# Optimization experiments

Hardware: AMD Instinct MI355X
Metric: run time of the kernel (lower is better)

## Reference

```python
import jax, jax.numpy as jnp
import numpy as np

TOLERANCE = 0.01  # init kwarg


def setup_inputs() -> dict:
    key = jax.random.key(0)
    k1, k2 = jax.random.split(key)
    B, N = 64, 2048
    logits = jax.random.normal(k1, (B, N), dtype=jnp.float32)
    labels = jax.random.uniform(k2, (B, N), dtype=jnp.float32)
    return {"logits": logits, "labels": labels}


def reference(logits, labels):
    # Original: for each row, sort labels descending; for every ordered pair
    # (high, low) in that order with |label_high - label_low| > tolerance,
    # accumulate log(sigmoid(logit_high - logit_low)); reduction='sum' per
    # row, then mean over the batch.
    # Vectorized equivalent: a pair contributes iff labels[a] - labels[b] > tol
    # (exactly one ordering per unordered pair, ties masked out).
    label_diff = labels[:, :, None] - labels[:, None, :]          # [B, N, N]
    mask = label_diff > TOLERANCE                                  # [B, N, N]
    logit_diff = logits[:, :, None] - logits[:, None, :]          # [B, N, N]
    log_sig = jax.nn.log_sigmoid(logit_diff)
    per_row = jnp.sum(jnp.where(mask, log_sig, 0.0), axis=(1, 2))  # [B]
    return jnp.mean(per_row)
```

## Files before the change

### kernel.cpp

```cpp
#include <hip/hip_runtime.h>
#include <math.h>


#define NN 2048
#define BB 64
#define TOLF 0.01f
#define BLK 256
#define NTILE 20
#define TILEBLKS (BB * NTILE)
#define SIDEBLKS (BB * 8)
#define WGRID (TILEBLKS + SIDEBLKS)
#define SWIN 448
#define LOG2E 1.4426950408889634f

typedef float v2f __attribute__((ext_vector_type(2)));

__device__ float2 g_labs[BB][NN];
__device__ float  g_Es[BB][NN];
__device__ int    g_C[BB][NN];
__device__ float  g_part[TILEBLKS];
__device__ double g_partS[SIDEBLKS];

__global__ __launch_bounds__(BLK) void rank_pre(const float* __restrict__ logits,
                                                const float* __restrict__ labels) {
    __shared__ float2 sls[NN];
    __shared__ float  sEv[NN];
    __shared__ int    sC[NN];
    __shared__ int    cnt[100], pref[101], offs[100];
    __shared__ int    wtot;
    const int row = blockIdx.x, tid = threadIdx.x;
    const float* lg = logits + (size_t)row * NN;
    const float* lb = labels + (size_t)row * NN;

    for (int x = tid; x < 100; x += BLK) { cnt[x] = 0; offs[x] = 0; }
    __syncthreads();

    int   myb[8];
    float myla[8], mylg[8];
#pragma unroll
    for (int q = 0; q < 8; ++q) {
        int x = tid + q * BLK;
        myla[q] = lb[x];
        mylg[q] = lg[x];
        myb[q]  = min(99, (int)(myla[q] * 100.0f));
        atomicAdd(&cnt[myb[q]], 1);
    }
    __syncthreads();
    {
        int v = (tid < 100) ? cnt[tid] : 0;
        int x = v;
#pragma unroll
        for (int o = 1; o < 64; o <<= 1) {
            int y = __shfl_up(x, o);
            if ((tid & 63) >= o) x += y;
        }
        if (tid == 63) wtot = x;
        __syncthreads();
        if (tid >= 64 && tid < 128) x += wtot;
        if (tid < 101) pref[tid] = x - v;
    }
    __syncthreads();
#pragma unroll
    for (int q = 0; q < 8; ++q) {
        int b = myb[q];
        int p = pref[b] + atomicAdd(&offs[b], 1);
        float s = mylg[q] * LOG2E;
        sls[p] = make_float2(myla[q], s);
        sEv[p] = __builtin_amdgcn_exp2f(s);
        sC[p]  = (b >= 1) ? pref[b - 1] : 0;
    }
    __syncthreads();
    for (int x = tid; x < NN; x += BLK) {
        g_labs[row][x] = sls[x];
        g_Es[row][x]   = sEv[x];
        g_C[row][x]    = sC[x];
    }
}

__global__ __launch_bounds__(BLK) void rank_work() {
    const int bid = blockIdx.x;
    if (bid < SIDEBLKS) {
        __shared__ float2 sLS[SWIN];
        __shared__ float  sE[SWIN];
        __shared__ int    sCs;
        __shared__ double sdw[4];
        const int row = bid >> 3;
        const int c0  = (bid & 7) << 8;
        const int tid = threadIdx.x;
        if (tid == 0) sCs = g_C[row][c0];
        __syncthreads();
        const int Cs  = sCs;
        const int len = c0 + 256 - Cs;
        for (int x = tid; x < len; x += BLK) {
            sLS[x] = g_labs[row][Cs + x];
            sE[x]  = g_Es[row][Cs + x];
        }
        __syncthreads();

        const int i    = c0 + tid;
        const int iloc = i - Cs;
        const float2 lsi = sLS[iloc];
        const float lai = lsi.x, si = lsi.y;
        const float Ei  = sE[iloc];
        const int wloc  = g_C[row][i] - Cs;

        float accL = 0.0f, accS = 0.0f;
        float p = 1.0f;
        int cnt8 = 0;
        for (int j = wloc; j < iloc; ++j) {
            float2 ls = sLS[j];
            float ld = lai - ls.x;
            bool valid = fabsf(ld) > TOLF;
            float term = valid ? (Ei + sE[j]) : 1.0f;
            p *= term;
            if (++cnt8 == 8) { accL += __builtin_amdgcn_logf(p); p = 1.0f; cnt8 = 0; }
            float sh = (ld > 0.0f) ? si : ls.y;
            accS -= valid ? sh : 0.0f;
        }
        accL += __builtin_amdgcn_logf(p);

        double acc = (double)accL + (double)accS;
        for (int off = 32; off > 0; off >>= 1) acc += __shfl_down(acc, off);
        if ((tid & 63) == 0) sdw[tid >> 6] = acc;
        __syncthreads();
        if (tid == 0) g_partS[bid] = sdw[0] + sdw[1] + sdw[2] + sdw[3];
    } else {
        __shared__ __align__(16) float swin[256];
        __shared__ float swave[4];
        const int tb = bid - SIDEBLKS;
        const int row = tb / NTILE;
        const int t = tb % NTILE;
        const int it = (t < 2) ? 0 : (t < 6) ? 1 : (t < 12) ? 2 : 3;
        const int jt = t - it * (it + 1);
        const int ibeg = it * 512, jbeg = jt * 256;

        float accL = 0.0f;
        const int Cmax = g_C[row][ibeg + 511];
        if (jbeg < Cmax) {
            for (int x = threadIdx.x; x < 64; x += BLK)
                ((float4*)swin)[x] = ((const float4*)&g_Es[row][jbeg])[x];
            __syncthreads();
            const int ia = ibeg + threadIdx.x;
            const int ib = ia + 256;
            const float invEa = __builtin_amdgcn_rcpf(g_Es[row][ia]);
            const float invEb = __builtin_amdgcn_rcpf(g_Es[row][ib]);
            v2f iA; iA.x = invEa; iA.y = invEa;
            v2f iB; iB.x = invEb; iB.y = invEb;
            int tripa = max(0, min(256, g_C[row][ia] - jbeg));
            int tripb = max(0, min(256, g_C[row][ib] - jbeg));
            const int m16a = tripa & ~15;
            const int m16b = tripb & ~15;

            for (int jj = 0; jj < m16a; jj += 16) {
                const v2f* qw = (const v2f*)&swin[jj];
                v2f a0; a0.x = 1.0f; a0.y = 1.0f;
                v2f a1 = a0, b0 = a0, b1 = a0;
#pragma unroll
                for (int u = 0; u < 4; ++u) {
                    v2f w = qw[u];
                    a0 = __builtin_elementwise_fma(w * iA, a0, a0);
                    b0 = __builtin_elementwise_fma(w * iB, b0, b0);
                }
#pragma unroll
                for (int u = 4; u < 8; ++u) {
                    v2f w = qw[u];
                    a1 = __builtin_elementwise_fma(w * iA, a1, a1);
                    b1 = __builtin_elementwise_fma(w * iB, b1, b1);
                }
                accL += __builtin_amdgcn_logf(a0.x * a0.y)
                      + __builtin_amdgcn_logf(a1.x * a1.y)
                      + __builtin_amdgcn_logf(b0.x * b0.y)
                      + __builtin_amdgcn_logf(b1.x * b1.y);
            }
            for (int jj = m16a; jj < m16b; jj += 16) {
                const v2f* qw = (const v2f*)&swin[jj];
                v2f b0; b0.x = 1.0f; b0.y = 1.0f;
                v2f b1 = b0;
#pragma unroll
                for (int u = 0; u < 4; ++u)
                    b0 = __builtin_elementwise_fma(qw[u] * iB, b0, b0);
#pragma unroll
                for (int u = 4; u < 8; ++u)
                    b1 = __builtin_elementwise_fma(qw[u] * iB, b1, b1);
                accL += __builtin_amdgcn_logf(b0.x * b0.y)
                      + __builtin_amdgcn_logf(b1.x * b1.y);
            }
            if (m16a < tripa) {
                float p0 = 1.0f, p1 = 1.0f;
#pragma unroll
                for (int u = 0; u < 8; ++u) {
                    float t0 = (m16a + u     < tripa) ? fmaf(swin[m16a + u],     invEa, 1.0f) : 1.0f;
                    float t1 = (m16a + 8 + u < tripa) ? fmaf(swin[m16a + 8 + u], invEa, 1.0f) : 1.0f;
                    p0 *= t0; p1 *= t1;
                }
                accL += __builtin_amdgcn_logf(p0) + __builtin_amdgcn_logf(p1);
            }
            if (m16b < tripb) {
                float p0 = 1.0f, p1 = 1.0f;
#pragma unroll
                for (int u = 0; u < 8; ++u) {
                    float t0 = (m16b + u     < tripb) ? fmaf(swin[m16b + u],     invEb, 1.0f) : 1.0f;
                    float t1 = (m16b + 8 + u < tripb) ? fmaf(swin[m16b + 8 + u], invEb, 1.0f) : 1.0f;
                    p0 *= t0; p1 *= t1;
                }
                accL += __builtin_amdgcn_logf(p0) + __builtin_amdgcn_logf(p1);
            }
        }
        for (int off = 32; off > 0; off >>= 1) accL += __shfl_down(accL, off);
        if ((threadIdx.x & 63) == 0) swave[threadIdx.x >> 6] = accL;
        __syncthreads();
        if (threadIdx.x == 0)
            g_part[tb] = swave[0] + swave[1] + swave[2] + swave[3];
    }
}

__global__ __launch_bounds__(BLK) void rank_final(float* __restrict__ out) {
    double acc = 0.0;
    for (int idx = threadIdx.x; idx < TILEBLKS; idx += BLK) acc += (double)g_part[idx];
    for (int idx = threadIdx.x; idx < SIDEBLKS; idx += BLK) acc += g_partS[idx];
    for (int off = 32; off > 0; off >>= 1) acc += __shfl_down(acc, off);
    __shared__ double sw[4];
    if ((threadIdx.x & 63) == 0) sw[threadIdx.x >> 6] = acc;
    __syncthreads();
    if (threadIdx.x == 0)
        out[0] = (float)((sw[0] + sw[1] + sw[2] + sw[3]) *
                         (-0.6931471805599453 / (double)BB));
}

extern "C" void kernel_launch(void* const* d_in, const int* in_sizes, int n_in,
                              void* d_out, int out_size, void* d_ws, size_t ws_size,
                              hipStream_t stream) {
    const float* logits = (const float*)d_in[0];
    const float* labels = (const float*)d_in[1];
    float* out = (float*)d_out;
    (void)in_sizes; (void)n_in; (void)out_size; (void)d_ws; (void)ws_size;

    rank_pre<<<BB, BLK, 0, stream>>>(logits, labels);
    rank_work<<<WGRID, BLK, 0, stream>>>();
    rank_final<<<1, BLK, 0, stream>>>(out);
}
```

Measured before the change: 26.64 us.

## Fuse preprocessing and pairwise work kernels with per-row ready flags

Merges the per-row bucket-sort preprocessing kernel and the pairwise work kernel into one launch. The first 64 blocks sort rows and publish a release flag, and worker blocks spin on that flag with acquire loads before processing. Each worker now handles two items in successive passes, and exp values and bucket starts are packed into a single float2 array to cut separate loads. This removes one launch gap and lets work overlap with preprocessing of other rows. It depends on the producer blocks being scheduled, which risks deadlock if resident capacity is exceeded, and it adds spin-wait overhead and halves worker parallelism.

```diff
diff --git a/kernel.cpp b/kernel.cpp
--- a/kernel.cpp
+++ b/kernel.cpp
@@ -9,208 +9,234 @@
 #define NTILE 20
 #define TILEBLKS (BB * NTILE)
 #define SIDEBLKS (BB * 8)
-#define WGRID (TILEBLKS + SIDEBLKS)
+#define NITEMS (TILEBLKS + SIDEBLKS)
+#define WBLKS (NITEMS / 2)
+#define GRID (BB + WBLKS)
 #define SWIN 448
 #define LOG2E 1.4426950408889634f
 
 typedef float v2f __attribute__((ext_vector_type(2)));
 
 __device__ float2 g_labs[BB][NN];
-__device__ float  g_Es[BB][NN];
-__device__ int    g_C[BB][NN];
+__device__ float2 g_EC[BB][NN];
+__device__ int    g_ready[BB * 16];
 __device__ float  g_part[TILEBLKS];
 __device__ double g_partS[SIDEBLKS];
 
-__global__ __launch_bounds__(BLK) void rank_pre(const float* __restrict__ logits,
-                                                const float* __restrict__ labels) {
-    __shared__ float2 sls[NN];
-    __shared__ float  sEv[NN];
-    __shared__ int    sC[NN];
-    __shared__ int    cnt[100], pref[101], offs[100];
-    __shared__ int    wtot;
-    const int row = blockIdx.x, tid = threadIdx.x;
-    const float* lg = logits + (size_t)row * NN;
-    const float* lb = labels + (size_t)row * NN;
-
-    for (int x = tid; x < 100; x += BLK) { cnt[x] = 0; offs[x] = 0; }
-    __syncthreads();
-
-    int   myb[8];
-    float myla[8], mylg[8];
-#pragma unroll
-    for (int q = 0; q < 8; ++q) {
-        int x = tid + q * BLK;
-        myla[q] = lb[x];
-        mylg[q] = lg[x];
-        myb[q]  = min(99, (int)(myla[q] * 100.0f));
-        atomicAdd(&cnt[myb[q]], 1);
+#define SMEM_BYTES 17664
+
+__global__ __launch_bounds__(BLK, 4) void rank_fused(const float* __restrict__ logits,
+                                                     const float* __restrict__ labels) {
+    __shared__ __align__(16) char smem[SMEM_BYTES];
+    const int bid = blockIdx.x, tid = threadIdx.x;
+
+    if (bid < BB) {
+        float2* st = (float2*)smem;
+        int* cnt  = (int*)(smem + 16384);
+        int* offs = cnt + 100;
+        int* pref = offs + 100;
+        int* wtot = pref + 101;
+        const int row = bid;
+        const float* lg = logits + (size_t)row * NN;
+        const float* lb = labels + (size_t)row * NN;
+
+        for (int x = tid; x < 100; x += BLK) { cnt[x] = 0; offs[x] = 0; }
+        __syncthreads();
+        float la8[8], lg8[8];
+        int   p8[8];
+#pragma unroll
+        for (int q = 0; q < 8; ++q) {
+            int x = tid + q * BLK;
+            la8[q] = lb[x];
+            lg8[q] = lg[x];
+            atomicAdd(&cnt[min(99, (int)(la8[q] * 100.0f))], 1);
+        }
+        __syncthreads();
+        {
+            int v = (tid < 100) ? cnt[tid] : 0;
+            int x = v;
+#pragma unroll
+            for (int o = 1; o < 64; o <<= 1) {
+                int y = __shfl_up(x, o);
+                if ((tid & 63) >= o) x += y;
+            }
+            if (tid == 63) *wtot = x;
+            __syncthreads();
+            if (tid >= 64 && tid < 128) x += *wtot;
+            if (tid < 101) pref[tid] = x - v;
+        }
+        __syncthreads();
+#pragma unroll
+        for (int q = 0; q < 8; ++q) {
+            int b = min(99, (int)(la8[q] * 100.0f));
+            p8[q] = pref[b] + atomicAdd(&offs[b], 1);
+            st[p8[q]] = make_float2(la8[q], lg8[q] * LOG2E);
+        }
+        __syncthreads();
+        for (int x = tid; x < NN; x += BLK) g_labs[row][x] = st[x];
+        __syncthreads();
+#pragma unroll
+        for (int q = 0; q < 8; ++q) {
+            int b = min(99, (int)(la8[q] * 100.0f));
+            float s = lg8[q] * LOG2E;
+            st[p8[q]] = make_float2(__builtin_amdgcn_exp2f(s),
+                                    __int_as_float((b >= 1) ? pref[b - 1] : 0));
+        }
+        __syncthreads();
+        for (int x = tid; x < NN; x += BLK) g_EC[row][x] = st[x];
+
+        __threadfence();
+        if (tid == 0)
+            __hip_atomic_store(&g_ready[row * 16], 1, __ATOMIC_RELEASE,
+                               __HIP_MEMORY_SCOPE_AGENT);
+        return;
     }
-    __syncthreads();
-    {
-        int v = (tid < 100) ? cnt[tid] : 0;
-        int x = v;
-#pragma unroll
-        for (int o = 1; o < 64; o <<= 1) {
-            int y = __shfl_up(x, o);
-            if ((tid & 63) >= o) x += y;
-        }
-        if (tid == 63) wtot = x;
-        __syncthreads();
-        if (tid >= 64 && tid < 128) x += wtot;
-        if (tid < 101) pref[tid] = x - v;
-    }
-    __syncthreads();
-#pragma unroll
-    for (int q = 0; q < 8; ++q) {
-        int b = myb[q];
-        int p = pref[b] + atomicAdd(&offs[b], 1);
-        float s = mylg[q] * LOG2E;
-        sls[p] = make_float2(myla[q], s);
-        sEv[p] = __builtin_amdgcn_exp2f(s);
-        sC[p]  = (b >= 1) ? pref[b - 1] : 0;
-    }
-    __syncthreads();
-    for (int x = tid; x < NN; x += BLK) {
-        g_labs[row][x] = sls[x];
-        g_Es[row][x]   = sEv[x];
-        g_C[row][x]    = sC[x];
-    }
-}
-
-__global__ __launch_bounds__(BLK) void rank_work() {
-    const int bid = blockIdx.x;
-    if (bid < SIDEBLKS) {
-        __shared__ float2 sLS[SWIN];
-        __shared__ float  sE[SWIN];
-        __shared__ int    sCs;
-        __shared__ double sdw[4];
-        const int row = bid >> 3;
-        const int c0  = (bid & 7) << 8;
-        const int tid = threadIdx.x;
-        if (tid == 0) sCs = g_C[row][c0];
-        __syncthreads();
-        const int Cs  = sCs;
-        const int len = c0 + 256 - Cs;
-        for (int x = tid; x < len; x += BLK) {
-            sLS[x] = g_labs[row][Cs + x];
-            sE[x]  = g_Es[row][Cs + x];
-        }
-        __syncthreads();
-
-        const int i    = c0 + tid;
-        const int iloc = i - Cs;
-        const float2 lsi = sLS[iloc];
-        const float lai = lsi.x, si = lsi.y;
-        const float Ei  = sE[iloc];
-        const int wloc  = g_C[row][i] - Cs;
-
-        float accL = 0.0f, accS = 0.0f;
-        float p = 1.0f;
-        int cnt8 = 0;
-        for (int j = wloc; j < iloc; ++j) {
-            float2 ls = sLS[j];
-            float ld = lai - ls.x;
-            bool valid = fabsf(ld) > TOLF;
-            float term = valid ? (Ei + sE[j]) : 1.0f;
-            p *= term;
-            if (++cnt8 == 8) { accL += __builtin_amdgcn_logf(p); p = 1.0f; cnt8 = 0; }
-            float sh = (ld > 0.0f) ? si : ls.y;
-            accS -= valid ? sh : 0.0f;
-        }
-        accL += __builtin_amdgcn_logf(p);
-
-        double acc = (double)accL + (double)accS;
-        for (int off = 32; off > 0; off >>= 1) acc += __shfl_down(acc, off);
-        if ((tid & 63) == 0) sdw[tid >> 6] = acc;
-        __syncthreads();
-        if (tid == 0) g_partS[bid] = sdw[0] + sdw[1] + sdw[2] + sdw[3];
-    } else {
-        __shared__ __align__(16) float swin[256];
-        __shared__ float swave[4];
-        const int tb = bid - SIDEBLKS;
-        const int row = tb / NTILE;
-        const int t = tb % NTILE;
-        const int it = (t < 2) ? 0 : (t < 6) ? 1 : (t < 12) ? 2 : 3;
-        const int jt = t - it * (it + 1);
-        const int ibeg = it * 512, jbeg = jt * 256;
-
-        float accL = 0.0f;
-        const int Cmax = g_C[row][ibeg + 511];
-        if (jbeg < Cmax) {
-            for (int x = threadIdx.x; x < 64; x += BLK)
-                ((float4*)swin)[x] = ((const float4*)&g_Es[row][jbeg])[x];
-            __syncthreads();
-            const int ia = ibeg + threadIdx.x;
-            const int ib = ia + 256;
-            const float invEa = __builtin_amdgcn_rcpf(g_Es[row][ia]);
-            const float invEb = __builtin_amdgcn_rcpf(g_Es[row][ib]);
-            v2f iA; iA.x = invEa; iA.y = invEa;
-            v2f iB; iB.x = invEb; iB.y = invEb;
-            int tripa = max(0, min(256, g_C[row][ia] - jbeg));
-            int tripb = max(0, min(256, g_C[row][ib] - jbeg));
-            const int m16a = tripa & ~15;
-            const int m16b = tripb & ~15;
-
-            for (int jj = 0; jj < m16a; jj += 16) {
-                const v2f* qw = (const v2f*)&swin[jj];
-                v2f a0; a0.x = 1.0f; a0.y = 1.0f;
-                v2f a1 = a0, b0 = a0, b1 = a0;
-#pragma unroll
-                for (int u = 0; u < 4; ++u) {
-                    v2f w = qw[u];
-                    a0 = __builtin_elementwise_fma(w * iA, a0, a0);
-                    b0 = __builtin_elementwise_fma(w * iB, b0, b0);
-                }
-#pragma unroll
-                for (int u = 4; u < 8; ++u) {
-                    v2f w = qw[u];
-                    a1 = __builtin_elementwise_fma(w * iA, a1, a1);
-                    b1 = __builtin_elementwise_fma(w * iB, b1, b1);
-                }
-                accL += __builtin_amdgcn_logf(a0.x * a0.y)
-                      + __builtin_amdgcn_logf(a1.x * a1.y)
-                      + __builtin_amdgcn_logf(b0.x * b0.y)
-                      + __builtin_amdgcn_logf(b1.x * b1.y);
-            }
-            for (int jj = m16a; jj < m16b; jj += 16) {
-                const v2f* qw = (const v2f*)&swin[jj];
-                v2f b0; b0.x = 1.0f; b0.y = 1.0f;
-                v2f b1 = b0;
-#pragma unroll
-                for (int u = 0; u < 4; ++u)
-                    b0 = __builtin_elementwise_fma(qw[u] * iB, b0, b0);
-#pragma unroll
-                for (int u = 4; u < 8; ++u)
-                    b1 = __builtin_elementwise_fma(qw[u] * iB, b1, b1);
-                accL += __builtin_amdgcn_logf(b0.x * b0.y)
-                      + __builtin_amdgcn_logf(b1.x * b1.y);
-            }
-            if (m16a < tripa) {
-                float p0 = 1.0f, p1 = 1.0f;
-#pragma unroll
-                for (int u = 0; u < 8; ++u) {
-                    float t0 = (m16a + u     < tripa) ? fmaf(swin[m16a + u],     invEa, 1.0f) : 1.0f;
-                    float t1 = (m16a + 8 + u < tripa) ? fmaf(swin[m16a + 8 + u], invEa, 1.0f) : 1.0f;
-                    p0 *= t0; p1 *= t1;
-                }
-                accL += __builtin_amdgcn_logf(p0) + __builtin_amdgcn_logf(p1);
-            }
-            if (m16b < tripb) {
-                float p0 = 1.0f, p1 = 1.0f;
-#pragma unroll
-                for (int u = 0; u < 8; ++u) {
-                    float t0 = (m16b + u     < tripb) ? fmaf(swin[m16b + u],     invEb, 1.0f) : 1.0f;
-                    float t1 = (m16b + 8 + u < tripb) ? fmaf(swin[m16b + 8 + u], invEb, 1.0f) : 1.0f;
-                    p0 *= t0; p1 *= t1;
-                }
-                accL += __builtin_amdgcn_logf(p0) + __builtin_amdgcn_logf(p1);
-            }
-        }
-        for (int off = 32; off > 0; off >>= 1) accL += __shfl_down(accL, off);
-        if ((threadIdx.x & 63) == 0) swave[threadIdx.x >> 6] = accL;
-        __syncthreads();
-        if (threadIdx.x == 0)
-            g_part[tb] = swave[0] + swave[1] + swave[2] + swave[3];
+
+    const int wb = bid - BB;
+    for (int pass = 0; pass < 2; ++pass) {
+        const int item = wb + pass * WBLKS;
+        const int row = (item < SIDEBLKS) ? (item >> 3)
+                                          : ((item - SIDEBLKS) / NTILE);
+        if (tid == 0) {
+            while (__hip_atomic_load(&g_ready[row * 16], __ATOMIC_ACQUIRE,
+                                     __HIP_MEMORY_SCOPE_AGENT) == 0)
+                __builtin_amdgcn_s_sleep(8);
+        }
+        __syncthreads();
+
+        if (item < SIDEBLKS) {
+            float2* sLS = (float2*)smem;
+            float*  sE  = (float*)(smem + 3584);
+            int*    sCs = (int*)(smem + 5376);
+            double* sdw = (double*)(smem + 5384);
+            const int c0 = (item & 7) << 8;
+            if (tid == 0) *sCs = __float_as_int(g_EC[row][c0].y);
+            __syncthreads();
+            const int Cs  = *sCs;
+            const int len = c0 + 256 - Cs;
+            for (int x = tid; x < len; x += BLK) {
+                sLS[x] = g_labs[row][Cs + x];
+                sE[x]  = g_EC[row][Cs + x].x;
+            }
+            __syncthreads();
+
+            const int i    = c0 + tid;
+            const int iloc = i - Cs;
+            const float2 lsi = sLS[iloc];
+            const float lai = lsi.x, si = lsi.y;
+            const float2 eci = g_EC[row][i];
+            const float Ei  = eci.x;
+            const int wloc  = __float_as_int(eci.y) - Cs;
+
+            float accL = 0.0f, accS = 0.0f;
+            float p = 1.0f;
+            int cnt8 = 0;
+            for (int j = wloc; j < iloc; ++j) {
+                float2 ls = sLS[j];
+                float ld = lai - ls.x;
+                bool valid = fabsf(ld) > TOLF;
+                float term = valid ? (Ei + sE[j]) : 1.0f;
+                p *= term;
+                if (++cnt8 == 8) { accL += __builtin_amdgcn_logf(p); p = 1.0f; cnt8 = 0; }
+                float sh = (ld > 0.0f) ? si : ls.y;
+                accS -= valid ? sh : 0.0f;
+            }
+            accL += __builtin_amdgcn_logf(p);
+
+            double acc = (double)accL + (double)accS;
+            for (int off = 32; off > 0; off >>= 1) acc += __shfl_down(acc, off);
+            if ((tid & 63) == 0) sdw[tid >> 6] = acc;
+            __syncthreads();
+            if (tid == 0) g_partS[item] = sdw[0] + sdw[1] + sdw[2] + sdw[3];
+            __syncthreads();
+        } else {
+            float* swin  = (float*)smem;
+            float* swave = (float*)(smem + 1024);
+            const int tb = item - SIDEBLKS;
+            const int t = tb % NTILE;
+            const int it = (t < 2) ? 0 : (t < 6) ? 1 : (t < 12) ? 2 : 3;
+            const int jt = t - it * (it + 1);
+            const int ibeg = it * 512, jbeg = jt * 256;
+
+            float accL = 0.0f;
+            const int Cmax = __float_as_int(g_EC[row][ibeg + 511].y);
+            if (jbeg < Cmax) {
+                swin[tid] = g_EC[row][jbeg + tid].x;
+                __syncthreads();
+                const int ia = ibeg + tid;
+                const int ib = ia + 256;
+                const float2 eca = g_EC[row][ia];
+                const float2 ecb = g_EC[row][ib];
+                const float invEa = __builtin_amdgcn_rcpf(eca.x);
+                const float invEb = __builtin_amdgcn_rcpf(ecb.x);
+                v2f iA; iA.x = invEa; iA.y = invEa;
+                v2f iB; iB.x = invEb; iB.y = invEb;
+                int tripa = max(0, min(256, __float_as_int(eca.y) - jbeg));
+                int tripb = max(0, min(256, __float_as_int(ecb.y) - jbeg));
+                const int m16a = tripa & ~15;
+                const int m16b = tripb & ~15;
+
+                for (int jj = 0; jj < m16a; jj += 16) {
+                    const v2f* qw = (const v2f*)&swin[jj];
+                    v2f a0; a0.x = 1.0f; a0.y = 1.0f;
+                    v2f a1 = a0, b0 = a0, b1 = a0;
+#pragma unroll
+                    for (int u = 0; u < 4; ++u) {
+                        v2f w = qw[u];
+                        a0 = __builtin_elementwise_fma(w * iA, a0, a0);
+                        b0 = __builtin_elementwise_fma(w * iB, b0, b0);
+                    }
+#pragma unroll
+                    for (int u = 4; u < 8; ++u) {
+                        v2f w = qw[u];
+                        a1 = __builtin_elementwise_fma(w * iA, a1, a1);
+                        b1 = __builtin_elementwise_fma(w * iB, b1, b1);
+                    }
+                    accL += __builtin_amdgcn_logf(a0.x * a0.y)
+                          + __builtin_amdgcn_logf(a1.x * a1.y)
+                          + __builtin_amdgcn_logf(b0.x * b0.y)
+                          + __builtin_amdgcn_logf(b1.x * b1.y);
+                }
+                for (int jj = m16a; jj < m16b; jj += 16) {
+                    const v2f* qw = (const v2f*)&swin[jj];
+                    v2f b0; b0.x = 1.0f; b0.y = 1.0f;
+                    v2f b1 = b0;
+#pragma unroll
+                    for (int u = 0; u < 4; ++u)
+                        b0 = __builtin_elementwise_fma(qw[u] * iB, b0, b0);
+#pragma unroll
+                    for (int u = 4; u < 8; ++u)
+                        b1 = __builtin_elementwise_fma(qw[u] * iB, b1, b1);
+                    accL += __builtin_amdgcn_logf(b0.x * b0.y)
+                          + __builtin_amdgcn_logf(b1.x * b1.y);
+                }
+                if (m16a < tripa) {
+                    float p0 = 1.0f, p1 = 1.0f;
+#pragma unroll
+                    for (int u = 0; u < 8; ++u) {
+                        float t0 = (m16a + u     < tripa) ? fmaf(swin[m16a + u],     invEa, 1.0f) : 1.0f;
+                        float t1 = (m16a + 8 + u < tripa) ? fmaf(swin[m16a + 8 + u], invEa, 1.0f) : 1.0f;
+                        p0 *= t0; p1 *= t1;
+                    }
+                    accL += __builtin_amdgcn_logf(p0) + __builtin_amdgcn_logf(p1);
+                }
+                if (m16b < tripb) {
+                    float p0 = 1.0f, p1 = 1.0f;
+#pragma unroll
+                    for (int u = 0; u < 8; ++u) {
+                        float t0 = (m16b + u     < tripb) ? fmaf(swin[m16b + u],     invEb, 1.0f) : 1.0f;
+                        float t1 = (m16b + 8 + u < tripb) ? fmaf(swin[m16b + 8 + u], invEb, 1.0f) : 1.0f;
+                        p0 *= t0; p1 *= t1;
+                    }
+                    accL += __builtin_amdgcn_logf(p0) + __builtin_amdgcn_logf(p1);
+                }
+            }
+            for (int off = 32; off > 0; off >>= 1) accL += __shfl_down(accL, off);
+            if ((tid & 63) == 0) swave[tid >> 6] = accL;
+            __syncthreads();
+            if (tid == 0) g_part[tb] = swave[0] + swave[1] + swave[2] + swave[3];
+            __syncthreads();
+        }
     }
 }
 
@@ -225,6 +251,7 @@
     if (threadIdx.x == 0)
         out[0] = (float)((sw[0] + sw[1] + sw[2] + sw[3]) *
                          (-0.6931471805599453 / (double)BB));
+    if (threadIdx.x < BB) g_ready[threadIdx.x * 16] = 0;
 }
 
 extern "C" void kernel_launch(void* const* d_in, const int* in_sizes, int n_in,
@@ -235,7 +262,6 @@
     float* out = (float*)d_out;
     (void)in_sizes; (void)n_in; (void)out_size; (void)d_ws; (void)ws_size;
 
-    rank_pre<<<BB, BLK, 0, stream>>>(logits, labels);
-    rank_work<<<WGRID, BLK, 0, stream>>>();
+    rank_fused<<<GRID, BLK, 0, stream>>>(logits, labels);
     rank_final<<<1, BLK, 0, stream>>>(out);
 }
```

Result: slower. 97.61 us (+266.4%).

## Split per-row bucket sort in rank_pre across eight blocks per row

Applied to the files above, without the earlier changes.

The preprocessing kernel now launches eight blocks per row instead of one. Each block redundantly loads the full label row and builds per-slice histograms, then uses per-slice prefix offsets to scatter only its own 256 elements directly to global memory. This raises parallelism from 64 blocks to 512 on a many-CU GPU, at the cost of redundant label loads and histogram work in every block and uncoalesced scattered global writes. The bucket order within a bin may differ from before, which is harmless for the pairwise sum.

```diff
diff --git a/kernel.cpp b/kernel.cpp
--- a/kernel.cpp
+++ b/kernel.cpp
@@ -10,6 +10,7 @@
 #define TILEBLKS (BB * NTILE)
 #define SIDEBLKS (BB * 8)
 #define WGRID (TILEBLKS + SIDEBLKS)
+#define PREBLKS (BB * 8)
 #define SWIN 448
 #define LOG2E 1.4426950408889634f
 
@@ -23,31 +24,38 @@
 
 __global__ __launch_bounds__(BLK) void rank_pre(const float* __restrict__ logits,
                                                 const float* __restrict__ labels) {
-    __shared__ float2 sls[NN];
-    __shared__ float  sEv[NN];
-    __shared__ int    sC[NN];
-    __shared__ int    cnt[100], pref[101], offs[100];
-    __shared__ int    wtot;
-    const int row = blockIdx.x, tid = threadIdx.x;
+    __shared__ float sLab[NN];
+    __shared__ int   hist[8][100];
+    __shared__ int   tot[100], before[100];
+    __shared__ int   pref[101], cursor[100];
+    __shared__ int   wtot;
+    const int bid = blockIdx.x;
+    const int row = bid >> 3;
+    const int slice = bid & 7;
+    const int tid = threadIdx.x;
     const float* lg = logits + (size_t)row * NN;
     const float* lb = labels + (size_t)row * NN;
 
-    for (int x = tid; x < 100; x += BLK) { cnt[x] = 0; offs[x] = 0; }
-    __syncthreads();
-
-    int   myb[8];
-    float myla[8], mylg[8];
+    for (int x = tid; x < 800; x += BLK) ((int*)hist)[x] = 0;
+    __syncthreads();
 #pragma unroll
     for (int q = 0; q < 8; ++q) {
-        int x = tid + q * BLK;
-        myla[q] = lb[x];
-        mylg[q] = lg[x];
-        myb[q]  = min(99, (int)(myla[q] * 100.0f));
-        atomicAdd(&cnt[myb[q]], 1);
+        int x = q * BLK + tid;
+        float la = lb[x];
+        sLab[x] = la;
+        atomicAdd(&hist[q][min(99, (int)(la * 100.0f))], 1);
+    }
+    __syncthreads();
+    if (tid < 100) {
+        int run = 0, bef = 0;
+#pragma unroll
+        for (int s = 0; s < 8; ++s) { if (s == slice) bef = run; run += hist[s][tid]; }
+        tot[tid] = run;
+        before[tid] = bef;
     }
     __syncthreads();
     {
-        int v = (tid < 100) ? cnt[tid] : 0;
+        int v = (tid < 100) ? tot[tid] : 0;
         int x = v;
 #pragma unroll
         for (int o = 1; o < 64; o <<= 1) {
@@ -60,20 +68,18 @@
         if (tid < 101) pref[tid] = x - v;
     }
     __syncthreads();
-#pragma unroll
-    for (int q = 0; q < 8; ++q) {
-        int b = myb[q];
-        int p = pref[b] + atomicAdd(&offs[b], 1);
-        float s = mylg[q] * LOG2E;
-        sls[p] = make_float2(myla[q], s);
-        sEv[p] = __builtin_amdgcn_exp2f(s);
-        sC[p]  = (b >= 1) ? pref[b - 1] : 0;
-    }
-    __syncthreads();
-    for (int x = tid; x < NN; x += BLK) {
-        g_labs[row][x] = sls[x];
-        g_Es[row][x]   = sEv[x];
-        g_C[row][x]    = sC[x];
+    if (tid < 100) cursor[tid] = pref[tid] + before[tid];
+    __syncthreads();
+    {
+        int x = (slice << 8) + tid;
+        float la  = sLab[x];
+        float lgx = lg[x];
+        int b = min(99, (int)(la * 100.0f));
+        int p = atomicAdd(&cursor[b], 1);
+        float s = lgx * LOG2E;
+        g_labs[row][p] = make_float2(la, s);
+        g_Es[row][p]   = __builtin_amdgcn_exp2f(s);
+        g_C[row][p]    = (b >= 1) ? pref[b - 1] : 0;
     }
 }
 
@@ -235,7 +241,7 @@
     float* out = (float*)d_out;
     (void)in_sizes; (void)n_in; (void)out_size; (void)d_ws; (void)ws_size;
 
-    rank_pre<<<BB, BLK, 0, stream>>>(logits, labels);
+    rank_pre<<<PREBLKS, BLK, 0, stream>>>(logits, labels);
     rank_work<<<WGRID, BLK, 0, stream>>>();
     rank_final<<<1, BLK, 0, stream>>>(out);
 }
```

Result: slower. 28.53 us (+7.1%).
